# Optimization experiments

Hardware: AMD Instinct MI355X
Metric: run time of the kernel (lower is better)

## Reference

```python
import jax, jax.numpy as jnp
import numpy as np

N_EMBD = 2048
N_HEAD = 8          # config.n_head // 2
HEAD_DIM = 256      # n_embd // (n_head // 2)
HALF = HEAD_DIM // 2
LAMBDA_INIT = 0.8
RMS_EPS = 1.1920929e-07  # torch float32 finfo eps (F.rms_norm default)


def _rms_norm(x):
    # F.rms_norm with no weight: x / sqrt(mean(x^2) + eps)
    return x * jax.lax.rsqrt(jnp.mean(x * x, axis=-1, keepdims=True) + RMS_EPS)


def setup_inputs() -> dict:
    key = jax.random.key(0)
    ks = jax.random.split(key, 10)
    B, T, C = 2, 2048, N_EMBD
    x = jax.random.normal(ks[0], (B, T, C), dtype=jnp.float32)
    wq = jax.random.normal(ks[1], (C, C), dtype=jnp.float32) * 0.02
    wk = jax.random.normal(ks[2], (C, C), dtype=jnp.float32) * 0.02
    wv = jax.random.normal(ks[3], (C, C), dtype=jnp.float32) * 0.02
    wo = jax.random.normal(ks[4], (C, C), dtype=jnp.float32) * 0.02
    lq1 = jax.random.normal(ks[5], (HEAD_DIM,), dtype=jnp.float32) * 0.1
    lk1 = jax.random.normal(ks[6], (HEAD_DIM,), dtype=jnp.float32) * 0.1
    lq2 = jax.random.normal(ks[7], (HEAD_DIM,), dtype=jnp.float32) * 0.1
    lk2 = jax.random.normal(ks[8], (HEAD_DIM,), dtype=jnp.float32) * 0.1
    return {"x": x, "wq": wq, "wk": wk, "wv": wv, "wo": wo,
            "lq1": lq1, "lk1": lk1, "lq2": lq2, "lk2": lk2}


def _causal_attn(q, k, v, mask):
    # q,k: [B,H,T,half], v: [B,H,T,HEAD_DIM]
    scale = 1.0 / jnp.sqrt(jnp.asarray(q.shape[-1], q.dtype))
    scores = jnp.einsum('bhqd,bhkd->bhqk', q, k) * scale
    scores = jnp.where(mask, scores, -jnp.inf)
    attn = jax.nn.softmax(scores, axis=-1)
    return jnp.einsum('bhqk,bhkd->bhqd', attn, v)


def reference(x, wq, wk, wv, wo, lq1, lk1, lq2, lk2):
    B, T, C = x.shape
    lambda_1 = jnp.exp(jnp.sum(lq1 * lk1))
    lambda_2 = jnp.exp(jnp.sum(lq2 * lk2))
    lambda_full = lambda_1 - lambda_2 + LAMBDA_INIT

    q = (x @ wq.T).reshape(B, T, N_HEAD, 2, HALF).transpose(0, 2, 1, 3, 4)  # [B,H,T,2,half]
    k = (x @ wk.T).reshape(B, T, N_HEAD, 2, HALF).transpose(0, 2, 1, 3, 4)
    v = (x @ wv.T).reshape(B, T, N_HEAD, HEAD_DIM).transpose(0, 2, 1, 3)    # [B,H,T,hd]

    q1 = _rms_norm(q[..., 0, :]); q2 = _rms_norm(q[..., 1, :])
    k1 = _rms_norm(k[..., 0, :]); k2 = _rms_norm(k[..., 1, :])

    mask = jnp.tril(jnp.ones((T, T), dtype=bool))
    y1 = _causal_attn(q1, k1, v, mask)
    y2 = _causal_attn(q2, k2, v, mask)
    y = y1 - lambda_full * y2                                               # [B,H,T,hd]

    y = y.transpose(0, 2, 1, 3).reshape(B, T, C)
    return (y @ wo.T) * (1.0 - LAMBDA_INIT)
```

## Files before the change

### kernel.cpp

```cpp
#include <hip/hip_runtime.h>
#include <stdint.h>


typedef __bf16 bf16;
typedef bf16 bf16x8 __attribute__((ext_vector_type(8)));
typedef bf16 bf16x4 __attribute__((ext_vector_type(4)));
typedef bf16 bf16x2 __attribute__((ext_vector_type(2)));
typedef float f32x4 __attribute__((ext_vector_type(4)));

typedef void __attribute__((address_space(1)))* gas_t;
typedef void __attribute__((address_space(3)))* las_t;

__device__ __forceinline__ void gload16(const void* g, void* l) {
  __builtin_amdgcn_global_load_lds((gas_t)(uintptr_t)g, (las_t)(uint32_t)(uintptr_t)l, 16, 0, 0);
}

__device__ __forceinline__ f32x4 mfma16x16(bf16x8 a, bf16x8 b, f32x4 c) {
  return __builtin_amdgcn_mfma_f32_16x16x32_bf16(a, b, c, 0, 0, 0);
}

__global__ __launch_bounds__(256) void cast_f32_bf16(const float* __restrict__ in,
                                                     bf16* __restrict__ out, int n4) {
  int i = blockIdx.x * 256 + threadIdx.x;
  if (i >= n4) return;
  float4 v = ((const float4*)in)[i];
  bf16x4 o;
  o[0] = (bf16)v.x; o[1] = (bf16)v.y; o[2] = (bf16)v.z; o[3] = (bf16)v.w;
  ((bf16x4*)out)[i] = o;
}

__global__ __launch_bounds__(256) void cast4_w(const float* __restrict__ a, const float* __restrict__ b,
                                               const float* __restrict__ c, const float* __restrict__ d,
                                               bf16* __restrict__ oa, bf16* __restrict__ ob,
                                               bf16* __restrict__ oc, bf16* __restrict__ od) {
  int w = blockIdx.y;
  const float* in = (w == 0) ? a : (w == 1) ? b : (w == 2) ? c : d;
  bf16* out = (w == 0) ? oa : (w == 1) ? ob : (w == 2) ? oc : od;
  int i = blockIdx.x * 256 + threadIdx.x;
  float4 v = ((const float4*)in)[i];
  bf16x4 o;
  o[0] = (bf16)v.x; o[1] = (bf16)v.y; o[2] = (bf16)v.z; o[3] = (bf16)v.w;
  ((bf16x4*)out)[i] = o;
}

__global__ void lambda_kernel(const float* __restrict__ lq1, const float* __restrict__ lk1,
                              const float* __restrict__ lq2, const float* __restrict__ lk2,
                              float* __restrict__ out) {
  __shared__ float red[8];
  int tid = threadIdx.x;
  float a = lq1[tid] * lk1[tid];
  float b = lq2[tid] * lk2[tid];
#pragma unroll
  for (int m = 32; m >= 1; m >>= 1) {
    a += __shfl_xor(a, m, 64);
    b += __shfl_xor(b, m, 64);
  }
  if ((tid & 63) == 0) { red[tid >> 6] = a; red[4 + (tid >> 6)] = b; }
  __syncthreads();
  if (tid == 0) {
    float s1 = red[0] + red[1] + red[2] + red[3];
    float s2 = red[4] + red[5] + red[6] + red[7];
    out[0] = expf(s1) - expf(s2) + 0.8f;
  }
}

__global__ __launch_bounds__(512, 2) void gemm_qkv8(const bf16* __restrict__ A,
                                                    const bf16* __restrict__ Bq,
                                                    const bf16* __restrict__ Bk,
                                                    const bf16* __restrict__ Bv,
                                                    bf16* __restrict__ Cq, bf16* __restrict__ Ck,
                                                    bf16* __restrict__ Cv) {
  __shared__ char lds[98304];
  const int K = 2048, nt = 64;

  int p = blockIdx.y * gridDim.x + blockIdx.x;
  int lid = (p & 7) * 48 + (p >> 3);
  const int bm = (lid / 24) * 256;
  const int bnG = (lid % 24) * 256;
  const int z = bnG >> 11;
  const int bn = bnG & 2047;
  const bf16* B = (z == 0) ? Bq : ((z == 1) ? Bk : Bv);

  const int tid = threadIdx.x;
  const int wid = tid >> 6, lane = tid & 63;
  const int l15 = lane & 15, lhi = lane >> 4;
  const int wm = wid >> 2, wn = wid & 3;

  const bf16* aS0 = A + (size_t)(bm + wid * 16 + l15) * K + lhi * 8;
  const bf16* bS0 = B + (size_t)(bn + wid * 16 + l15) * K + lhi * 8;

  auto stA = [&](int t, int pb) {
    char* d = lds + pb * 32768 + wid * 1024;
    const bf16* s = aS0 + t * 32;
    gload16(s, d);
    gload16(s + (size_t)128 * K, d + 8192);
  };
  auto stB = [&](int t, int pb) {
    char* d = lds + pb * 32768 + 16384 + wid * 1024;
    const bf16* s = bS0 + t * 32;
    gload16(s, d);
    gload16(s + (size_t)128 * K, d + 8192);
  };

  const f32x4 fz = {0.f, 0.f, 0.f, 0.f};
  f32x4 acc[8][4];
#pragma unroll
  for (int m = 0; m < 8; ++m)
#pragma unroll
    for (int n = 0; n < 4; ++n) acc[m][n] = fz;

  stA(0, 0); stB(0, 0);
  stA(1, 1); stB(1, 1);
  asm volatile("s_waitcnt vmcnt(4)" ::: "memory");
  __builtin_amdgcn_s_barrier();

  int cur = 0;
  for (int t = 0; t < nt; ++t) {
    const char* ab = lds + cur * 32768;
    const char* bb = ab + 16384;
    int nx2 = cur + 2; if (nx2 >= 3) nx2 -= 3;
    bf16x8 a[8], b0, b1;

#pragma unroll
    for (int m = 0; m < 8; ++m) a[m] = *(const bf16x8*)(ab + (wm * 8 + m) * 1024 + lane * 16);
    b0 = *(const bf16x8*)(bb + (wn * 4 + 0) * 1024 + lane * 16);
    b1 = *(const bf16x8*)(bb + (wn * 4 + 1) * 1024 + lane * 16);
    if (t + 2 < nt) stA(t + 2, nx2);
    __builtin_amdgcn_s_barrier();
    __builtin_amdgcn_s_setprio(1);
#pragma unroll
    for (int m = 0; m < 8; ++m) {
      acc[m][0] = mfma16x16(a[m], b0, acc[m][0]);
      acc[m][1] = mfma16x16(a[m], b1, acc[m][1]);
    }
    __builtin_amdgcn_s_setprio(0);
    __builtin_amdgcn_s_barrier();

    b0 = *(const bf16x8*)(bb + (wn * 4 + 2) * 1024 + lane * 16);
    b1 = *(const bf16x8*)(bb + (wn * 4 + 3) * 1024 + lane * 16);
    if (t + 2 < nt) stB(t + 2, nx2);
    __builtin_amdgcn_s_barrier();
    __builtin_amdgcn_s_setprio(1);
#pragma unroll
    for (int m = 0; m < 8; ++m) {
      acc[m][2] = mfma16x16(a[m], b0, acc[m][2]);
      acc[m][3] = mfma16x16(a[m], b1, acc[m][3]);
    }
    __builtin_amdgcn_s_setprio(0);
    if (t + 2 < nt) {
      asm volatile("s_waitcnt vmcnt(4)" ::: "memory");
    } else {
      asm volatile("s_waitcnt vmcnt(0)" ::: "memory");
    }
    __builtin_amdgcn_s_barrier();

    cur = (cur == 2) ? 0 : cur + 1;
  }

  if (z == 2) {
#pragma unroll
    for (int m = 0; m < 8; ++m)
#pragma unroll
      for (int n = 0; n < 4; ++n)
#pragma unroll
        for (int r = 0; r < 4; ++r) {
          int row = bm + wm * 128 + m * 16 + lhi * 4 + r;
          int col = bn + wn * 64 + n * 16 + l15;
          int bb3 = row >> 11, tt = row & 2047;
          Cv[(size_t)bb3 * 2048 * 2048 + (size_t)col * 2048 + tt] = (bf16)acc[m][n][r];
        }
    return;
  }
  float* ldsf = (float*)lds;
#pragma unroll
  for (int m = 0; m < 8; ++m)
#pragma unroll
    for (int r = 0; r < 4; ++r) {
      float s = acc[m][0][r] * acc[m][0][r] + acc[m][1][r] * acc[m][1][r] +
                acc[m][2][r] * acc[m][2][r] + acc[m][3][r] * acc[m][3][r];
      s += __shfl_xor(s, 1, 64);
      s += __shfl_xor(s, 2, 64);
      s += __shfl_xor(s, 4, 64);
      s += __shfl_xor(s, 8, 64);
      if (l15 == 0) ldsf[(wm * 128 + m * 16 + lhi * 4 + r) * 4 + wn] = s;
    }
  __syncthreads();
  const float osc = (z == 0) ? 0.08838834764831845f : 1.0f;
  bf16* C = (z == 0) ? Cq : Ck;
#pragma unroll
  for (int m = 0; m < 8; ++m) {
#pragma unroll
    for (int r = 0; r < 4; ++r) {
      int rl = wm * 128 + m * 16 + lhi * 4 + r;
      float tot = ldsf[rl * 4 + (wn & 2)] + ldsf[rl * 4 + (wn & 2) + 1];
      float sc = rsqrtf(tot * (1.0f / 128.0f) + 1.1920929e-07f) * osc;
#pragma unroll
      for (int n = 0; n < 4; ++n) {
        int col = bn + wn * 64 + n * 16 + l15;
        C[(size_t)(bm + rl) * 2048 + col] = (bf16)(acc[m][n][r] * sc);
      }
    }
  }
}

__global__ __launch_bounds__(512) void gemm_out(const bf16* __restrict__ A, const bf16* __restrict__ B,
                                                float* __restrict__ Cf) {
  __shared__ char lds[73728];
  const int K = 2048, nt = 64;

  int p = blockIdx.x;
  int lid = (p & 7) * 32 + (p >> 3);
  const int bm = (lid >> 4) * 256;
  const int bn = (lid & 15) * 128;

  const int tid = threadIdx.x;
  const int wid = tid >> 6, lane = tid & 63;
  const int l15 = lane & 15, lhi = lane >> 4;
  const int wm = wid >> 1, wn = wid & 1;

  const bf16* aB = A + (size_t)(bm + wid * 16 + l15) * K + lhi * 8;
  const bf16* bB = B + (size_t)(bn + wid * 16 + l15) * K + lhi * 8;

  auto stage = [&](int t, int pb) {
    char* base = lds + pb * 24576;
    const int k0 = t * 32;
    gload16(aB + k0, base + wid * 1024);
    gload16(aB + (size_t)128 * K + k0, base + 8192 + wid * 1024);
    gload16(bB + k0, base + 16384 + wid * 1024);
  };

  const f32x4 fz = {0.f, 0.f, 0.f, 0.f};
  f32x4 acc[4][4];
#pragma unroll
  for (int m = 0; m < 4; ++m)
#pragma unroll
    for (int n = 0; n < 4; ++n) acc[m][n] = fz;

  stage(0, 0);
  stage(1, 1);
  asm volatile("s_waitcnt vmcnt(3)" ::: "memory");
  __builtin_amdgcn_s_barrier();

  for (int t = 0; t < nt; ++t) {
    const char* ab = lds + (t % 3) * 24576;
    if (t + 2 < nt) stage(t + 2, (t + 2) % 3);
    bf16x8 a[4], b[4];
#pragma unroll
    for (int m = 0; m < 4; ++m)
      a[m] = *(const bf16x8*)(ab + (wm * 4 + m) * 1024 + lane * 16);
#pragma unroll
    for (int n = 0; n < 4; ++n)
      b[n] = *(const bf16x8*)(ab + 16384 + (wn * 4 + n) * 1024 + lane * 16);
    __builtin_amdgcn_s_setprio(1);
#pragma unroll
    for (int m = 0; m < 4; ++m)
#pragma unroll
      for (int n = 0; n < 4; ++n) acc[m][n] = mfma16x16(a[m], b[n], acc[m][n]);
    __builtin_amdgcn_s_setprio(0);
    if (t + 2 < nt) {
      asm volatile("s_waitcnt vmcnt(3)" ::: "memory");
    } else {
      asm volatile("s_waitcnt vmcnt(0)" ::: "memory");
    }
    __builtin_amdgcn_s_barrier();
  }

#pragma unroll
  for (int m = 0; m < 4; ++m)
#pragma unroll
    for (int n = 0; n < 4; ++n)
#pragma unroll
      for (int r = 0; r < 4; ++r) {
        int row = bm + wm * 64 + m * 16 + lhi * 4 + r;
        int col = bn + wn * 64 + n * 16 + l15;
        Cf[(size_t)row * 2048 + col] = acc[m][n][r] * 0.2f;
      }
}

__global__ __launch_bounds__(256) void attn_kernel(const bf16* __restrict__ qb, const bf16* __restrict__ kb,
                                                   const bf16* __restrict__ vtb, bf16* __restrict__ yb,
                                                   const float* __restrict__ lamp) {
  __shared__ char lds[73728];
  const int tid = threadIdx.x;
  const int wid = tid >> 6, lane = tid & 63;
  const int l15 = lane & 15, lhi = lane >> 4;
  char* pl = lds + 65536 + wid * 2048;
  const int s = wid >> 1;
  const int rg = wid & 1;

  const int p = blockIdx.x;
  const int bh = p & 15;
  const int qt = (p < 256) ? (31 - (p >> 4)) : ((p - 256) >> 4);
  const int b = bh >> 3, h = bh & 7;
  const int wr0 = qt * 64 + rg * 32;
  const float lam = lamp[0];

  bf16x8 qf[2][4];
#pragma unroll
  for (int rf = 0; rf < 2; ++rf) {
    const bf16* qrow = qb + (size_t)(b * 2048 + wr0 + rf * 16 + l15) * 2048 + h * 256 + s * 128 + lhi * 8;
#pragma unroll
    for (int c = 0; c < 4; ++c) qf[rf][c] = *(const bf16x8*)(qrow + c * 32);
  }

  const f32x4 fz = {0.f, 0.f, 0.f, 0.f};
  f32x4 y[2][16];
#pragma unroll
  for (int rf = 0; rf < 2; ++rf)
#pragma unroll
    for (int f = 0; f < 16; ++f) y[rf][f] = fz;
  float lsum[2][4] = {{0.f, 0.f, 0.f, 0.f}, {0.f, 0.f, 0.f, 0.f}};

  const int nkt = 2 * qt + 2;
  const bf16* kbase = kb + (size_t)(b * 2048) * 2048 + h * 256;
  const bf16* vbase = vtb + (size_t)b * 2048 * 2048 + (size_t)(h * 256) * 2048;

  auto stageK = [&](int kt2, int pp) {
    const int t0 = kt2 * 32;
    char* kd = lds + pp * 16384 + wid * 1024;
    const bf16* sp = kbase + (size_t)(t0 + l15) * 2048 + wid * 32 + lhi * 8;
    gload16(sp, kd);
    gload16(sp + 16 * 2048, kd + 4096);
    gload16(sp + 128, kd + 8192);
    gload16(sp + 16 * 2048 + 128, kd + 12288);
  };
  auto stageVT = [&](int kt2, int pp) {
    const int t0 = kt2 * 32;
    char* vd = lds + 32768 + pp * 16384;
    const bf16* vp = vbase + (size_t)(wid * 16 + l15) * 2048 + t0 + lhi * 8;
#pragma unroll
    for (int i = 0; i < 4; ++i)
      gload16(vp + (size_t)i * 64 * 2048, vd + (i * 4 + wid) * 1024);
  };

  stageK(0, 0);
  stageVT(0, 0);
  __syncthreads();

  for (int kt = 0; kt < nkt; ++kt) {
    const int cur = kt & 1;
    const int t0 = kt * 32;
    const bool active = (t0 <= wr0 + 31);
    if (kt + 1 < nkt) {
      stageK(kt + 1, cur ^ 1);
      stageVT(kt + 1, cur ^ 1);
    }
    if (active) {
      const char* kc = lds + cur * 16384 + s * 8192;
      const char* vc = lds + 32768 + cur * 16384;
      f32x4 sg[2][2];
      __builtin_amdgcn_s_setprio(1);
#pragma unroll
      for (int rf = 0; rf < 2; ++rf)
#pragma unroll
        for (int g = 0; g < 2; ++g) {
          f32x4 a = fz;
#pragma unroll
          for (int ks = 0; ks < 4; ++ks)
            a = mfma16x16(qf[rf][ks], *(const bf16x8*)(kc + ((g * 4 + ks) * 64 + lane) * 16), a);
          sg[rf][g] = a;
        }
      __builtin_amdgcn_s_setprio(0);
      if (t0 + 31 > wr0) {
#pragma unroll
        for (int rf = 0; rf < 2; ++rf)
#pragma unroll
          for (int g = 0; g < 2; ++g) {
            int col = t0 + g * 16 + l15;
#pragma unroll
            for (int r = 0; r < 4; ++r) {
              int row = wr0 + rf * 16 + lhi * 4 + r;
              if (col > row) sg[rf][g][r] = -1e30f;
            }
          }
      }
#pragma unroll
      for (int rf = 0; rf < 2; ++rf)
#pragma unroll
        for (int g = 0; g < 2; ++g)
#pragma unroll
          for (int r = 0; r < 4; ++r) {
            float pv = __expf(sg[rf][g][r] - 12.0f);
            lsum[rf][r] += pv;
            *(bf16*)(pl + rf * 1024 + ((lhi * 4 + r) * 32 + g * 16 + l15) * 2) = (bf16)pv;
          }
      bf16x8 pa0 = *(const bf16x8*)(pl + (l15 * 32 + lhi * 8) * 2);
      bf16x8 pa1 = *(const bf16x8*)(pl + 1024 + (l15 * 32 + lhi * 8) * 2);
      __builtin_amdgcn_s_setprio(1);
#pragma unroll
      for (int f = 0; f < 16; ++f) {
        bf16x8 vf = *(const bf16x8*)(vc + (f * 64 + lane) * 16);
        y[0][f] = mfma16x16(pa0, vf, y[0][f]);
        y[1][f] = mfma16x16(pa1, vf, y[1][f]);
      }
      __builtin_amdgcn_s_setprio(0);
    }
    __syncthreads();
  }

  float inv[2][4];
#pragma unroll
  for (int rf = 0; rf < 2; ++rf)
#pragma unroll
    for (int r = 0; r < 4; ++r) {
      float sv = lsum[rf][r];
      sv += __shfl_xor(sv, 1, 64);
      sv += __shfl_xor(sv, 2, 64);
      sv += __shfl_xor(sv, 4, 64);
      sv += __shfl_xor(sv, 8, 64);
      inv[rf][r] = (s == 0) ? (1.f / sv) : (lam / sv);
    }
  float* yx = (float*)lds;
  if (s == 0) {
#pragma unroll
    for (int rf = 0; rf < 2; ++rf)
#pragma unroll
      for (int f = 0; f < 16; ++f)
#pragma unroll
        for (int r = 0; r < 4; ++r) {
          int rl = rg * 32 + rf * 16 + lhi * 4 + r;
          yx[rl * 256 + f * 16 + l15] = y[rf][f][r] * inv[rf][r];
        }
  }
  __syncthreads();
  if (s == 1) {
#pragma unroll
    for (int rf = 0; rf < 2; ++rf)
#pragma unroll
      for (int r = 0; r < 4; ++r) {
        int rl = rg * 32 + rf * 16 + lhi * 4 + r;
        bf16* orow = yb + (size_t)(b * 2048 + qt * 64 + rl) * 2048 + h * 256 + l15;
#pragma unroll
        for (int f = 0; f < 16; ++f) {
          float v = yx[rl * 256 + f * 16 + l15] - y[rf][f][r] * inv[rf][r];
          orow[f * 16] = (bf16)v;
        }
      }
  }
}

extern "C" void kernel_launch(void* const* d_in, const int* in_sizes, int n_in,
                              void* d_out, int out_size, void* d_ws, size_t ws_size,
                              hipStream_t stream) {
  const float* x = (const float*)d_in[0];
  const float* wq = (const float*)d_in[1];
  const float* wk = (const float*)d_in[2];
  const float* wv = (const float*)d_in[3];
  const float* wo = (const float*)d_in[4];
  const float* lq1 = (const float*)d_in[5];
  const float* lk1 = (const float*)d_in[6];
  const float* lq2 = (const float*)d_in[7];
  const float* lk2 = (const float*)d_in[8];
  float* out = (float*)d_out;
  char* ws = (char*)d_ws;

  if (ws_size < 117440516) return;

  bf16* xb = (bf16*)(ws + 0);
  bf16* wqb = (bf16*)(ws + 16777216);
  bf16* wkb = (bf16*)(ws + 25165824);
  bf16* wvb = (bf16*)(ws + 33554432);
  bf16* wob = (bf16*)(ws + 41943040);
  bf16* qbuf = (bf16*)(ws + 50331648);
  bf16* kbuf = (bf16*)(ws + 67108864);
  bf16* vtb = (bf16*)(ws + 83886080);
  bf16* ybuf = (bf16*)(ws + 100663296);
  float* lam = (float*)(ws + 117440512);

  cast_f32_bf16<<<8192, 256, 0, stream>>>(x, xb, 2097152);
  cast4_w<<<dim3(4096, 4), 256, 0, stream>>>(wq, wk, wv, wo, wqb, wkb, wvb, wob);
  lambda_kernel<<<1, 256, 0, stream>>>(lq1, lk1, lq2, lk2, lam);

  gemm_qkv8<<<dim3(24, 16), 512, 0, stream>>>(xb, wqb, wkb, wvb, qbuf, kbuf, vtb);

  attn_kernel<<<512, 256, 0, stream>>>(qbuf, kbuf, vtb, ybuf, lam);

  gemm_out<<<256, 512, 0, stream>>>(ybuf, wob, out);
}
```

Measured before the change: 343.2 us.

## Fuse cast/lambda kernels and use single-buffered 64-key attention tiles

Result: slower. 398.3 us (+16.0%).

```diff
diff --git a/kernel.cpp b/kernel.cpp
--- a/kernel.cpp
+++ b/kernel.cpp
@@ -5,7 +5,6 @@
 typedef __bf16 bf16;
 typedef bf16 bf16x8 __attribute__((ext_vector_type(8)));
 typedef bf16 bf16x4 __attribute__((ext_vector_type(4)));
-typedef bf16 bf16x2 __attribute__((ext_vector_type(2)));
 typedef float f32x4 __attribute__((ext_vector_type(4)));
 
 typedef void __attribute__((address_space(1)))* gas_t;
@@ -19,48 +18,50 @@
   return __builtin_amdgcn_mfma_f32_16x16x32_bf16(a, b, c, 0, 0, 0);
 }
 
-__global__ __launch_bounds__(256) void cast_f32_bf16(const float* __restrict__ in,
-                                                     bf16* __restrict__ out, int n4) {
-  int i = blockIdx.x * 256 + threadIdx.x;
-  if (i >= n4) return;
-  float4 v = ((const float4*)in)[i];
+__global__ __launch_bounds__(256) void cast_all(const float* __restrict__ x,
+                                                const float* __restrict__ wq, const float* __restrict__ wk,
+                                                const float* __restrict__ wv, const float* __restrict__ wo,
+                                                const float* __restrict__ lq1, const float* __restrict__ lk1,
+                                                const float* __restrict__ lq2, const float* __restrict__ lk2,
+                                                bf16* __restrict__ xb,
+                                                bf16* __restrict__ wqb, bf16* __restrict__ wkb,
+                                                bf16* __restrict__ wvb, bf16* __restrict__ wob,
+                                                float* __restrict__ lam) {
+  __shared__ float red[8];
+  int tid = threadIdx.x;
+  int i = blockIdx.x * 256 + tid;
+  const float* in;
+  bf16* out;
+  int j;
+  if (i < 2097152) {
+    in = x; out = xb; j = i;
+  } else {
+    int k = i - 2097152;
+    int w = k >> 20;
+    j = k & 1048575;
+    in = (w == 0) ? wq : (w == 1) ? wk : (w == 2) ? wv : wo;
+    out = (w == 0) ? wqb : (w == 1) ? wkb : (w == 2) ? wvb : wob;
+  }
+  float4 v = ((const float4*)in)[j];
   bf16x4 o;
   o[0] = (bf16)v.x; o[1] = (bf16)v.y; o[2] = (bf16)v.z; o[3] = (bf16)v.w;
-  ((bf16x4*)out)[i] = o;
-}
-
-__global__ __launch_bounds__(256) void cast4_w(const float* __restrict__ a, const float* __restrict__ b,
-                                               const float* __restrict__ c, const float* __restrict__ d,
-                                               bf16* __restrict__ oa, bf16* __restrict__ ob,
-                                               bf16* __restrict__ oc, bf16* __restrict__ od) {
-  int w = blockIdx.y;
-  const float* in = (w == 0) ? a : (w == 1) ? b : (w == 2) ? c : d;
-  bf16* out = (w == 0) ? oa : (w == 1) ? ob : (w == 2) ? oc : od;
-  int i = blockIdx.x * 256 + threadIdx.x;
-  float4 v = ((const float4*)in)[i];
-  bf16x4 o;
-  o[0] = (bf16)v.x; o[1] = (bf16)v.y; o[2] = (bf16)v.z; o[3] = (bf16)v.w;
-  ((bf16x4*)out)[i] = o;
-}
-
-__global__ void lambda_kernel(const float* __restrict__ lq1, const float* __restrict__ lk1,
-                              const float* __restrict__ lq2, const float* __restrict__ lk2,
-                              float* __restrict__ out) {
-  __shared__ float red[8];
-  int tid = threadIdx.x;
-  float a = lq1[tid] * lk1[tid];
-  float b = lq2[tid] * lk2[tid];
-#pragma unroll
-  for (int m = 32; m >= 1; m >>= 1) {
-    a += __shfl_xor(a, m, 64);
-    b += __shfl_xor(b, m, 64);
-  }
-  if ((tid & 63) == 0) { red[tid >> 6] = a; red[4 + (tid >> 6)] = b; }
-  __syncthreads();
-  if (tid == 0) {
-    float s1 = red[0] + red[1] + red[2] + red[3];
-    float s2 = red[4] + red[5] + red[6] + red[7];
-    out[0] = expf(s1) - expf(s2) + 0.8f;
+  ((bf16x4*)out)[j] = o;
+
+  if (blockIdx.x == 0) {
+    float a = lq1[tid] * lk1[tid];
+    float b = lq2[tid] * lk2[tid];
+#pragma unroll
+    for (int m = 32; m >= 1; m >>= 1) {
+      a += __shfl_xor(a, m, 64);
+      b += __shfl_xor(b, m, 64);
+    }
+    if ((tid & 63) == 0) { red[tid >> 6] = a; red[4 + (tid >> 6)] = b; }
+    __syncthreads();
+    if (tid == 0) {
+      float s1 = red[0] + red[1] + red[2] + red[3];
+      float s2 = red[4] + red[5] + red[6] + red[7];
+      lam[0] = expf(s1) - expf(s2) + 0.8f;
+    }
   }
 }
 
@@ -280,11 +281,12 @@
 __global__ __launch_bounds__(256) void attn_kernel(const bf16* __restrict__ qb, const bf16* __restrict__ kb,
                                                    const bf16* __restrict__ vtb, bf16* __restrict__ yb,
                                                    const float* __restrict__ lamp) {
-  __shared__ char lds[73728];
+  __shared__ char lds[81920];
   const int tid = threadIdx.x;
   const int wid = tid >> 6, lane = tid & 63;
   const int l15 = lane & 15, lhi = lane >> 4;
-  char* pl = lds + 65536 + wid * 2048;
+  char* vtl = lds + 32768;
+  char* pl = lds + 65536 + wid * 4096;
   const int s = wid >> 1;
   const int rg = wid & 1;
 
@@ -311,91 +313,102 @@
     for (int f = 0; f < 16; ++f) y[rf][f] = fz;
   float lsum[2][4] = {{0.f, 0.f, 0.f, 0.f}, {0.f, 0.f, 0.f, 0.f}};
 
-  const int nkt = 2 * qt + 2;
+  const int nkt = qt + 1;
   const bf16* kbase = kb + (size_t)(b * 2048) * 2048 + h * 256;
   const bf16* vbase = vtb + (size_t)b * 2048 * 2048 + (size_t)(h * 256) * 2048;
 
-  auto stageK = [&](int kt2, int pp) {
-    const int t0 = kt2 * 32;
-    char* kd = lds + pp * 16384 + wid * 1024;
-    const bf16* sp = kbase + (size_t)(t0 + l15) * 2048 + wid * 32 + lhi * 8;
-    gload16(sp, kd);
-    gload16(sp + 16 * 2048, kd + 4096);
-    gload16(sp + 128, kd + 8192);
-    gload16(sp + 16 * 2048 + 128, kd + 12288);
+  auto stage = [&](int kt2) {
+    const int t0 = kt2 * 64;
+#pragma unroll
+    for (int c = 0; c < 8; ++c) {
+      int cc = wid * 8 + c;
+      int ss = cc >> 4, tg = (cc >> 2) & 3, kc = cc & 3;
+      const bf16* sp = kbase + (size_t)(t0 + tg * 16 + l15) * 2048 + ss * 128 + kc * 32 + lhi * 8;
+      gload16(sp, lds + ss * 16384 + (tg * 4 + kc) * 1024);
+    }
+#pragma unroll
+    for (int c = 0; c < 8; ++c) {
+      int cc = wid * 8 + c;
+      int f = cc >> 1, ks = cc & 1;
+      const bf16* vp = vbase + (size_t)(f * 16 + l15) * 2048 + t0 + ks * 32 + lhi * 8;
+      gload16(vp, vtl + f * 2048 + ks * 1024);
+    }
   };
-  auto stageVT = [&](int kt2, int pp) {
-    const int t0 = kt2 * 32;
-    char* vd = lds + 32768 + pp * 16384;
-    const bf16* vp = vbase + (size_t)(wid * 16 + l15) * 2048 + t0 + lhi * 8;
-#pragma unroll
-    for (int i = 0; i < 4; ++i)
-      gload16(vp + (size_t)i * 64 * 2048, vd + (i * 4 + wid) * 1024);
-  };
-
-  stageK(0, 0);
-  stageVT(0, 0);
+
+  stage(0);
   __syncthreads();
 
   for (int kt = 0; kt < nkt; ++kt) {
-    const int cur = kt & 1;
-    const int t0 = kt * 32;
-    const bool active = (t0 <= wr0 + 31);
+    const int t0 = kt * 64;
+    const bool diag = (kt == qt);
+    const bool upper = diag && (rg == 0);
+    const char* kc0 = lds + s * 16384;
+
+    f32x4 sg[2][4];
+    __builtin_amdgcn_s_setprio(1);
+#pragma unroll
+    for (int rf = 0; rf < 2; ++rf)
+#pragma unroll
+      for (int g = 0; g < 4; ++g) {
+        f32x4 a = fz;
+        if (!(upper && g >= 2)) {
+#pragma unroll
+          for (int kc = 0; kc < 4; ++kc)
+            a = mfma16x16(qf[rf][kc], *(const bf16x8*)(kc0 + (g * 4 + kc) * 1024 + lane * 16), a);
+        }
+        sg[rf][g] = a;
+      }
+    __builtin_amdgcn_s_setprio(0);
+    if (diag) {
+#pragma unroll
+      for (int rf = 0; rf < 2; ++rf)
+#pragma unroll
+        for (int g = 0; g < 4; ++g) {
+          int col = t0 + g * 16 + l15;
+#pragma unroll
+          for (int r = 0; r < 4; ++r) {
+            int row = wr0 + rf * 16 + lhi * 4 + r;
+            if (col > row) sg[rf][g][r] = -1e30f;
+          }
+        }
+    }
+#pragma unroll
+    for (int rf = 0; rf < 2; ++rf)
+#pragma unroll
+      for (int g = 0; g < 4; ++g)
+#pragma unroll
+        for (int r = 0; r < 4; ++r) {
+          float pv = __expf(sg[rf][g][r] - 12.0f);
+          lsum[rf][r] += pv;
+          int row = lhi * 4 + r;
+          int byte = row * 128 + (g * 16 + l15) * 2;
+          *(bf16*)(pl + rf * 2048 + (byte ^ ((row & 7) << 4))) = (bf16)pv;
+        }
+    bf16x8 pa[2][2];
+#pragma unroll
+    for (int rf = 0; rf < 2; ++rf)
+#pragma unroll
+      for (int ks = 0; ks < 2; ++ks) {
+        int byte = l15 * 128 + ks * 64 + lhi * 16;
+        pa[rf][ks] = *(const bf16x8*)(pl + rf * 2048 + (byte ^ ((l15 & 7) << 4)));
+      }
+    __builtin_amdgcn_s_setprio(1);
+#pragma unroll
+    for (int f = 0; f < 16; ++f)
+#pragma unroll
+      for (int ks = 0; ks < 2; ++ks) {
+        if (upper && ks == 1) continue;
+        bf16x8 vf = *(const bf16x8*)(vtl + f * 2048 + ks * 1024 + lane * 16);
+        y[0][f] = mfma16x16(pa[0][ks], vf, y[0][f]);
+        y[1][f] = mfma16x16(pa[1][ks], vf, y[1][f]);
+      }
+    __builtin_amdgcn_s_setprio(0);
+
+    __syncthreads();
     if (kt + 1 < nkt) {
-      stageK(kt + 1, cur ^ 1);
-      stageVT(kt + 1, cur ^ 1);
-    }
-    if (active) {
-      const char* kc = lds + cur * 16384 + s * 8192;
-      const char* vc = lds + 32768 + cur * 16384;
-      f32x4 sg[2][2];
-      __builtin_amdgcn_s_setprio(1);
-#pragma unroll
-      for (int rf = 0; rf < 2; ++rf)
-#pragma unroll
-        for (int g = 0; g < 2; ++g) {
-          f32x4 a = fz;
-#pragma unroll
-          for (int ks = 0; ks < 4; ++ks)
-            a = mfma16x16(qf[rf][ks], *(const bf16x8*)(kc + ((g * 4 + ks) * 64 + lane) * 16), a);
-          sg[rf][g] = a;
-        }
-      __builtin_amdgcn_s_setprio(0);
-      if (t0 + 31 > wr0) {
-#pragma unroll
-        for (int rf = 0; rf < 2; ++rf)
-#pragma unroll
-          for (int g = 0; g < 2; ++g) {
-            int col = t0 + g * 16 + l15;
-#pragma unroll
-            for (int r = 0; r < 4; ++r) {
-              int row = wr0 + rf * 16 + lhi * 4 + r;
-              if (col > row) sg[rf][g][r] = -1e30f;
-            }
-          }
-      }
-#pragma unroll
-      for (int rf = 0; rf < 2; ++rf)
-#pragma unroll
-        for (int g = 0; g < 2; ++g)
-#pragma unroll
-          for (int r = 0; r < 4; ++r) {
-            float pv = __expf(sg[rf][g][r] - 12.0f);
-            lsum[rf][r] += pv;
-            *(bf16*)(pl + rf * 1024 + ((lhi * 4 + r) * 32 + g * 16 + l15) * 2) = (bf16)pv;
-          }
-      bf16x8 pa0 = *(const bf16x8*)(pl + (l15 * 32 + lhi * 8) * 2);
-      bf16x8 pa1 = *(const bf16x8*)(pl + 1024 + (l15 * 32 + lhi * 8) * 2);
-      __builtin_amdgcn_s_setprio(1);
-#pragma unroll
-      for (int f = 0; f < 16; ++f) {
-        bf16x8 vf = *(const bf16x8*)(vc + (f * 64 + lane) * 16);
-        y[0][f] = mfma16x16(pa0, vf, y[0][f]);
-        y[1][f] = mfma16x16(pa1, vf, y[1][f]);
-      }
-      __builtin_amdgcn_s_setprio(0);
-    }
-    __syncthreads();
+      stage(kt + 1);
+      __syncthreads();
+    }
   }
 
   float inv[2][4];
@@ -467,9 +480,8 @@
   bf16* ybuf = (bf16*)(ws + 100663296);
   float* lam = (float*)(ws + 117440512);
 
-  cast_f32_bf16<<<8192, 256, 0, stream>>>(x, xb, 2097152);
-  cast4_w<<<dim3(4096, 4), 256, 0, stream>>>(wq, wk, wv, wo, wqb, wkb, wvb, wob);
-  lambda_kernel<<<1, 256, 0, stream>>>(lq1, lk1, lq2, lk2, lam);
+  cast_all<<<24576, 256, 0, stream>>>(x, wq, wk, wv, wo, lq1, lk1, lq2, lk2,
+                                      xb, wqb, wkb, wvb, wob, lam);
 
   gemm_qkv8<<<dim3(24, 16), 512, 0, stream>>>(xb, wqb, wkb, wvb, qbuf, kbuf, vtb);
 
```
